# Kernel optimization log

Hardware: AMD Instinct MI355X
Metric: run time of the kernel (lower is better)

The kernel has to match this reference:

```python
import jax, jax.numpy as jnp
import numpy as np

I = 1024
H = 1024
B = 4096
EPS = 1e-5

def layer_norm(x, gamma, beta):
    mu = jnp.mean(x, axis=-1, keepdims=True)
    var = jnp.var(x, axis=-1, keepdims=True)
    return (x - mu) * jax.lax.rsqrt(var + EPS) * gamma + beta

def setup_inputs() -> dict:
    key = jax.random.key(0)
    ks = jax.random.split(key, 5)
    return {
        "input": jax.random.normal(ks[0], (B, I), dtype=jnp.float32),
        "hx": jax.random.normal(ks[1], (B, H), dtype=jnp.float32),
        "cx": jax.random.normal(ks[2], (B, H), dtype=jnp.float32),
        "weight_ih": jax.random.normal(ks[3], (4 * H, I), dtype=jnp.float32),
        "weight_hh": jax.random.normal(ks[4], (4 * H, H), dtype=jnp.float32),
        "gamma_i": jnp.ones((4 * H,), jnp.float32),
        "beta_i": jnp.zeros((4 * H,), jnp.float32),
        "gamma_h": jnp.ones((4 * H,), jnp.float32),
        "beta_h": jnp.zeros((4 * H,), jnp.float32),
        "gamma_c": jnp.ones((H,), jnp.float32),
        "beta_c": jnp.zeros((H,), jnp.float32),
    }

def reference(input, hx, cx, weight_ih, weight_hh,
              gamma_i, beta_i, gamma_h, beta_h, gamma_c, beta_c):
    # igates: [B, 4H]
    igates = layer_norm(jnp.dot(input, weight_ih.T), gamma_i, beta_i)
    hgates = layer_norm(jnp.dot(hx, weight_hh.T), gamma_h, beta_h)
    gates = igates + hgates
    ingate, forgetgate, cellgate, outgate = jnp.split(gates, 4, axis=1)
    ingate = jax.nn.sigmoid(ingate)
    forgetgate = jax.nn.sigmoid(forgetgate)
    cellgate = jnp.tanh(cellgate)
    outgate = jax.nn.sigmoid(outgate)
    cy = layer_norm(forgetgate * cx + ingate * cellgate, gamma_c, beta_c)
    hy = outgate * jnp.tanh(cy)
    return (hy, hy, cy)
```

## Files before the change

kernel.cpp:

```cpp
#include <hip/hip_runtime.h>

#define EPS 1e-5f

typedef unsigned short u16;
typedef __attribute__((ext_vector_type(8))) __bf16 bf16x8;
typedef __attribute__((ext_vector_type(4))) float f32x4;
typedef __attribute__((ext_vector_type(8))) unsigned short ushort8;

__device__ inline float bf2f(u16 h) {
  union { unsigned u; float f; } x; x.u = ((unsigned)h) << 16; return x.f;
}
__device__ inline u16 f2bf(float f) {
  union { float f; unsigned u; } x; x.f = f;
  unsigned r = x.u + 0x7fffu + ((x.u >> 16) & 1u);
  return (u16)(r >> 16);
}
__device__ inline float sigmoidf(float x) { return 1.0f / (1.0f + __expf(-x)); }

__global__ __launch_bounds__(256) void cast4_f32_bf16(
    const float* __restrict__ s0, const float* __restrict__ s1,
    const float* __restrict__ s2, const float* __restrict__ s3,
    u16* __restrict__ d0, u16* __restrict__ d1,
    u16* __restrict__ d2, u16* __restrict__ d3, int n)
{
  const float* s = (blockIdx.y == 0) ? s0 : (blockIdx.y == 1) ? s1 : (blockIdx.y == 2) ? s2 : s3;
  u16*         d = (blockIdx.y == 0) ? d0 : (blockIdx.y == 1) ? d1 : (blockIdx.y == 2) ? d2 : d3;
  int i = (blockIdx.x * 256 + threadIdx.x) * 8;
  if (i >= n) return;
  float4 a = *(const float4*)(s + i);
  float4 b = *(const float4*)(s + i + 4);
  ushort8 o;
  o[0] = f2bf(a.x); o[1] = f2bf(a.y); o[2] = f2bf(a.z); o[3] = f2bf(a.w);
  o[4] = f2bf(b.x); o[5] = f2bf(b.y); o[6] = f2bf(b.z); o[7] = f2bf(b.w);
  *(ushort8*)(d + i) = o;
}

#define MFMA_ __builtin_amdgcn_mfma_f32_16x16x32_bf16

#define STAGE_A(nx, k0) { _Pragma("unroll") for (int i_ = 0; i_ < 4; ++i_) \
  __builtin_amdgcn_global_load_lds( \
      (const __attribute__((address_space(1))) void*)(gA + (size_t)(i_ * 64) * K + (k0)), \
      (__attribute__((address_space(3))) void*)(&sA[nx][(i_ * 512 + (w << 6)) * 8]), 16, 0, 0); }
#define STAGE_B(nx, k0) { _Pragma("unroll") for (int i_ = 0; i_ < 4; ++i_) \
  __builtin_amdgcn_global_load_lds( \
      (const __attribute__((address_space(1))) void*)(gB + (size_t)(i_ * 64) * K + (k0)), \
      (__attribute__((address_space(3))) void*)(&sB[nx][(i_ * 512 + (w << 6)) * 8]), 16, 0, 0); }

#define LDA(mi, sl) (*(const bf16x8*)&sa[(arow + (mi) * 16) * 64 + (sl)])
#define LDB(ni, sl) (*(const bf16x8*)&sb[(brow + (ni) * 16) * 64 + (sl)])

#define MFMA16(m0) \
  __builtin_amdgcn_s_setprio(1); \
  acc[m0 + 0][0] = MFMA_(a0, q0, acc[m0 + 0][0], 0, 0, 0); \
  acc[m0 + 0][1] = MFMA_(a0, q1, acc[m0 + 0][1], 0, 0, 0); \
  acc[m0 + 0][2] = MFMA_(a0, q2, acc[m0 + 0][2], 0, 0, 0); \
  acc[m0 + 0][3] = MFMA_(a0, q3, acc[m0 + 0][3], 0, 0, 0); \
  acc[m0 + 1][0] = MFMA_(a1, q0, acc[m0 + 1][0], 0, 0, 0); \
  acc[m0 + 1][1] = MFMA_(a1, q1, acc[m0 + 1][1], 0, 0, 0); \
  acc[m0 + 1][2] = MFMA_(a1, q2, acc[m0 + 1][2], 0, 0, 0); \
  acc[m0 + 1][3] = MFMA_(a1, q3, acc[m0 + 1][3], 0, 0, 0); \
  acc[m0 + 2][0] = MFMA_(a2, q0, acc[m0 + 2][0], 0, 0, 0); \
  acc[m0 + 2][1] = MFMA_(a2, q1, acc[m0 + 2][1], 0, 0, 0); \
  acc[m0 + 2][2] = MFMA_(a2, q2, acc[m0 + 2][2], 0, 0, 0); \
  acc[m0 + 2][3] = MFMA_(a2, q3, acc[m0 + 2][3], 0, 0, 0); \
  acc[m0 + 3][0] = MFMA_(a3, q0, acc[m0 + 3][0], 0, 0, 0); \
  acc[m0 + 3][1] = MFMA_(a3, q1, acc[m0 + 3][1], 0, 0, 0); \
  acc[m0 + 3][2] = MFMA_(a3, q2, acc[m0 + 3][2], 0, 0, 0); \
  acc[m0 + 3][3] = MFMA_(a3, q3, acc[m0 + 3][3], 0, 0, 0); \
  __builtin_amdgcn_s_setprio(0);

#define PHASE(m0, sl, RB) { \
  bf16x8 a0 = LDA(m0 + 0, sl), a1 = LDA(m0 + 1, sl), a2 = LDA(m0 + 2, sl), a3 = LDA(m0 + 3, sl); \
  if (RB) { q0 = LDB(0, sl); q1 = LDB(1, sl); q2 = LDB(2, sl); q3 = LDB(3, sl); } \
  __builtin_amdgcn_s_barrier(); \
  MFMA16(m0) }

#define PHASE_NOBAR(m0, sl, RB) { \
  bf16x8 a0 = LDA(m0 + 0, sl), a1 = LDA(m0 + 1, sl), a2 = LDA(m0 + 2, sl), a3 = LDA(m0 + 3, sl); \
  if (RB) { q0 = LDB(0, sl); q1 = LDB(1, sl); q2 = LDB(2, sl); q3 = LDB(3, sl); } \
  MFMA16(m0) }

__global__ __launch_bounds__(512, 2) void gemm256_dual(
    const u16* __restrict__ A0, const u16* __restrict__ W0, u16* __restrict__ C0,
    const u16* __restrict__ A1, const u16* __restrict__ W1, u16* __restrict__ C1)
{
  constexpr int K = 1024, N = 4096, NT = 16;

  __shared__ __attribute__((aligned(16))) u16 sA[2][256 * 64];
  __shared__ __attribute__((aligned(16))) u16 sB[2][256 * 64];

  const int b0  = blockIdx.x;
  const int bid = (b0 & 7) * 64 + (b0 >> 3);

  const u16* A  = (bid < 256) ? A0 : A1;
  const u16* Wm = (bid < 256) ? W0 : W1;
  u16*       C  = (bid < 256) ? C0 : C1;
  const int b2 = bid & 255;
  const int bm = (b2 >> 4) << 8;
  const int bn = (b2 & 15) << 8;

  const int tid = threadIdx.x;
  const int l  = tid & 63;
  const int w  = tid >> 6;
  const int wr = w >> 2;
  const int wc = w & 3;

  const int rb   = tid >> 3;
  const int slot = (tid & 7) ^ (rb & 7);
  const u16* gA = A  + (size_t)(bm + rb) * K + slot * 8;
  const u16* gB = Wm + (size_t)(bn + rb) * K + slot * 8;

  const int arow = wr * 128 + (l & 15);
  const int brow = wc * 64 + (l & 15);
  const int sl0 = (((l >> 4) + 0) ^ (l & 7)) * 8;
  const int sl1 = (((l >> 4) + 4) ^ (l & 7)) * 8;

  f32x4 acc[8][4];
#pragma unroll
  for (int i = 0; i < 8; ++i)
#pragma unroll
    for (int j = 0; j < 4; ++j) acc[i][j] = (f32x4){0.f, 0.f, 0.f, 0.f};

  STAGE_A(0, 0)
  STAGE_B(0, 0)

  for (int t = 0; t < NT - 1; ++t) {
    const int cur = t & 1, nxt = cur ^ 1;
    const int kn = (t + 1) << 6;
    const u16* sa = sA[cur];
    const u16* sb = sB[cur];
    bf16x8 q0, q1, q2, q3;

    STAGE_A(nxt, kn)
    asm volatile("s_waitcnt vmcnt(4)" ::: "memory");
    __builtin_amdgcn_s_barrier();
    PHASE_NOBAR(0, sl0, 1)
    __builtin_amdgcn_s_barrier();
    STAGE_B(nxt, kn)
    PHASE(4, sl0, 0)
    __builtin_amdgcn_s_barrier();
    PHASE(0, sl1, 1)
    __builtin_amdgcn_s_barrier();
    PHASE(4, sl1, 0)
  }

  {
    const u16* sa = sA[(NT - 1) & 1];
    const u16* sb = sB[(NT - 1) & 1];
    bf16x8 q0, q1, q2, q3;
    asm volatile("s_waitcnt vmcnt(0)" ::: "memory");
    __builtin_amdgcn_s_barrier();
    PHASE_NOBAR(0, sl0, 1)
    __builtin_amdgcn_s_barrier();
    PHASE(4, sl0, 0)
    __builtin_amdgcn_s_barrier();
    PHASE(0, sl1, 1)
    __builtin_amdgcn_s_barrier();
    PHASE(4, sl1, 0)
  }

  const int ccol = bn + wc * 64 + (l & 15);
  const int crow = bm + wr * 128 + (l >> 4) * 4;
#pragma unroll
  for (int mi = 0; mi < 8; ++mi) {
#pragma unroll
    for (int ni = 0; ni < 4; ++ni) {
      int col = ccol + ni * 16;
#pragma unroll
      for (int r = 0; r < 4; ++r) {
        int row = crow + mi * 16 + r;
        C[(size_t)row * N + col] = f2bf(acc[mi][ni][r]);
      }
    }
  }
}

__global__ __launch_bounds__(256) void lstm_epilogue(
    const u16* __restrict__ ig, const u16* __restrict__ hg,
    const float* __restrict__ cx,
    const float* __restrict__ gi, const float* __restrict__ bi,
    const float* __restrict__ gh, const float* __restrict__ bh,
    const float* __restrict__ gc, const float* __restrict__ bc,
    float* __restrict__ out)
{
  const int b = blockIdx.x;
  const int t = threadIdx.x;
  const u16* igr = ig + (size_t)b * 4096;
  const u16* hgr = hg + (size_t)b * 4096;

  __shared__ float redbuf[16];

  float iv[16], hv[16];
  float s_i = 0.f, q_i = 0.f, s_h = 0.f, q_h = 0.f;
#pragma unroll
  for (int i = 0; i < 16; ++i) {
    float a = bf2f(igr[t + 256 * i]);
    float c = bf2f(hgr[t + 256 * i]);
    iv[i] = a; hv[i] = c;
    s_i += a; q_i += a * a; s_h += c; q_h += c * c;
  }
#pragma unroll
  for (int off = 32; off > 0; off >>= 1) {
    s_i += __shfl_xor(s_i, off);
    q_i += __shfl_xor(q_i, off);
    s_h += __shfl_xor(s_h, off);
    q_h += __shfl_xor(q_h, off);
  }
  {
    int wv = t >> 6;
    if ((t & 63) == 0) {
      redbuf[wv] = s_i; redbuf[wv + 4] = q_i;
      redbuf[wv + 8] = s_h; redbuf[wv + 12] = q_h;
    }
    __syncthreads();
    s_i = redbuf[0] + redbuf[1] + redbuf[2] + redbuf[3];
    q_i = redbuf[4] + redbuf[5] + redbuf[6] + redbuf[7];
    s_h = redbuf[8] + redbuf[9] + redbuf[10] + redbuf[11];
    q_h = redbuf[12] + redbuf[13] + redbuf[14] + redbuf[15];
    __syncthreads();
  }
  const float inv4096 = 1.0f / 4096.0f;
  float mu_i = s_i * inv4096;
  float rs_i = rsqrtf(q_i * inv4096 - mu_i * mu_i + EPS);
  float mu_h = s_h * inv4096;
  float rs_h = rsqrtf(q_h * inv4096 - mu_h * mu_h + EPS);

  float c_pre[4], og[4];
  float s_c = 0.f, q_c = 0.f;
#pragma unroll
  for (int i = 0; i < 4; ++i) {
    int h = t + 256 * i;
    float g_in = ((iv[i]      - mu_i) * rs_i * gi[h]        + bi[h]) +
                 ((hv[i]      - mu_h) * rs_h * gh[h]        + bh[h]);
    float g_fg = ((iv[i + 4]  - mu_i) * rs_i * gi[h + 1024] + bi[h + 1024]) +
                 ((hv[i + 4]  - mu_h) * rs_h * gh[h + 1024] + bh[h + 1024]);
    float g_cl = ((iv[i + 8]  - mu_i) * rs_i * gi[h + 2048] + bi[h + 2048]) +
                 ((hv[i + 8]  - mu_h) * rs_h * gh[h + 2048] + bh[h + 2048]);
    float g_og = ((iv[i + 12] - mu_i) * rs_i * gi[h + 3072] + bi[h + 3072]) +
                 ((hv[i + 12] - mu_h) * rs_h * gh[h + 3072] + bh[h + 3072]);
    float in_s = sigmoidf(g_in);
    float fg_s = sigmoidf(g_fg);
    float cl_t = tanhf(g_cl);
    og[i] = sigmoidf(g_og);
    c_pre[i] = fg_s * cx[(size_t)b * 1024 + h] + in_s * cl_t;
    s_c += c_pre[i]; q_c += c_pre[i] * c_pre[i];
  }
#pragma unroll
  for (int off = 32; off > 0; off >>= 1) {
    s_c += __shfl_xor(s_c, off);
    q_c += __shfl_xor(q_c, off);
  }
  {
    int wv = t >> 6;
    if ((t & 63) == 0) { redbuf[wv] = s_c; redbuf[wv + 4] = q_c; }
    __syncthreads();
    s_c = redbuf[0] + redbuf[1] + redbuf[2] + redbuf[3];
    q_c = redbuf[4] + redbuf[5] + redbuf[6] + redbuf[7];
  }
  const float inv1024 = 1.0f / 1024.0f;
  float mu_c = s_c * inv1024;
  float rs_c = rsqrtf(q_c * inv1024 - mu_c * mu_c + EPS);

  const size_t BH = (size_t)4096 * 1024;
#pragma unroll
  for (int i = 0; i < 4; ++i) {
    int h = t + 256 * i;
    float cy = (c_pre[i] - mu_c) * rs_c * gc[h] + bc[h];
    float hy = og[i] * tanhf(cy);
    size_t o = (size_t)b * 1024 + h;
    out[o] = hy;
    out[BH + o] = hy;
    out[2 * BH + o] = cy;
  }
}

extern "C" void kernel_launch(void* const* d_in, const int* in_sizes, int n_in,
                              void* d_out, int out_size, void* d_ws, size_t ws_size,
                              hipStream_t stream) {
  const float* input = (const float*)d_in[0];
  const float* hx    = (const float*)d_in[1];
  const float* cx    = (const float*)d_in[2];
  const float* wih   = (const float*)d_in[3];
  const float* whh   = (const float*)d_in[4];
  const float* gi    = (const float*)d_in[5];
  const float* bi    = (const float*)d_in[6];
  const float* gh    = (const float*)d_in[7];
  const float* bh    = (const float*)d_in[8];
  const float* gc    = (const float*)d_in[9];
  const float* bc    = (const float*)d_in[10];
  float* out = (float*)d_out;

  char* wsp = (char*)d_ws;
  u16* a_bf  = (u16*)(wsp);
  u16* h_bf  = (u16*)(wsp + ((size_t)8  << 20));
  u16* wi_bf = (u16*)(wsp + ((size_t)16 << 20));
  u16* wh_bf = (u16*)(wsp + ((size_t)24 << 20));
  u16* ig_bf = (u16*)(wsp + ((size_t)32 << 20));
  u16* hg_bf = (u16*)(wsp + ((size_t)64 << 20));

  const int nper = 4096 * 1024;
  dim3 cgrid(nper / 8 / 256, 4);
  cast4_f32_bf16<<<cgrid, 256, 0, stream>>>(input, hx, wih, whh,
                                            a_bf, h_bf, wi_bf, wh_bf, nper);

  gemm256_dual<<<512, 512, 0, stream>>>(a_bf, wi_bf, ig_bf,
                                        h_bf, wh_bf, hg_bf);

  lstm_epilogue<<<4096, 256, 0, stream>>>(ig_bf, hg_bf, cx,
                                          gi, bi, gh, bh, gc, bc, out);
}
```

Before: 125.2 us.

## Halve GEMM K-tile to 32 and restructure staging/compute phases for higher occupancy

The K tile of the dual bf16 GEMM shrinks from 64 to 32, which halves LDS usage per block and doubles the iteration count. Staging of A and B is merged into one macro with a new XOR swizzle for the 32-wide rows. Each iteration now issues its MFMAs in two halves with a single barrier instead of four barrier-separated phases. The launch bound is raised to 4 blocks per CU to get more occupancy and latency hiding, at the cost of register pressure and more loop overhead per FLOP.

```diff
diff --git a/kernel.cpp b/kernel.cpp
--- a/kernel.cpp
+++ b/kernel.cpp
@@ -37,19 +37,20 @@
 
 #define MFMA_ __builtin_amdgcn_mfma_f32_16x16x32_bf16
 
-#define STAGE_A(nx, k0) { _Pragma("unroll") for (int i_ = 0; i_ < 4; ++i_) \
-  __builtin_amdgcn_global_load_lds( \
-      (const __attribute__((address_space(1))) void*)(gA + (size_t)(i_ * 64) * K + (k0)), \
-      (__attribute__((address_space(3))) void*)(&sA[nx][(i_ * 512 + (w << 6)) * 8]), 16, 0, 0); }
-#define STAGE_B(nx, k0) { _Pragma("unroll") for (int i_ = 0; i_ < 4; ++i_) \
-  __builtin_amdgcn_global_load_lds( \
-      (const __attribute__((address_space(1))) void*)(gB + (size_t)(i_ * 64) * K + (k0)), \
-      (__attribute__((address_space(3))) void*)(&sB[nx][(i_ * 512 + (w << 6)) * 8]), 16, 0, 0); }
-
-#define LDA(mi, sl) (*(const bf16x8*)&sa[(arow + (mi) * 16) * 64 + (sl)])
-#define LDB(ni, sl) (*(const bf16x8*)&sb[(brow + (ni) * 16) * 64 + (sl)])
-
-#define MFMA16(m0) \
+#define STAGE(nx, kt) { \
+  _Pragma("unroll") for (int i_ = 0; i_ < 2; ++i_) \
+    __builtin_amdgcn_global_load_lds( \
+        (const __attribute__((address_space(1))) void*)(gA + (size_t)(i_ * 128) * K + (kt)), \
+        (__attribute__((address_space(3))) void*)(&sA[nx][(i_ * 512 + tid) * 8]), 16, 0, 0); \
+  _Pragma("unroll") for (int i_ = 0; i_ < 2; ++i_) \
+    __builtin_amdgcn_global_load_lds( \
+        (const __attribute__((address_space(1))) void*)(gB + (size_t)(i_ * 128) * K + (kt)), \
+        (__attribute__((address_space(3))) void*)(&sB[nx][(i_ * 512 + tid) * 8]), 16, 0, 0); }
+
+#define LDA(mi) (*(const bf16x8*)&sa[(arow + (mi) * 16) * 32 + slr])
+#define LDB(ni) (*(const bf16x8*)&sb[(brow + (ni) * 16) * 32 + slr])
+
+#define MFMA16(m0, a0, a1, a2, a3) \
   __builtin_amdgcn_s_setprio(1); \
   acc[m0 + 0][0] = MFMA_(a0, q0, acc[m0 + 0][0], 0, 0, 0); \
   acc[m0 + 0][1] = MFMA_(a0, q1, acc[m0 + 0][1], 0, 0, 0); \
@@ -69,25 +70,22 @@
   acc[m0 + 3][3] = MFMA_(a3, q3, acc[m0 + 3][3], 0, 0, 0); \
   __builtin_amdgcn_s_setprio(0);
 
-#define PHASE(m0, sl, RB) { \
-  bf16x8 a0 = LDA(m0 + 0, sl), a1 = LDA(m0 + 1, sl), a2 = LDA(m0 + 2, sl), a3 = LDA(m0 + 3, sl); \
-  if (RB) { q0 = LDB(0, sl); q1 = LDB(1, sl); q2 = LDB(2, sl); q3 = LDB(3, sl); } \
+#define TILE_COMPUTE(sa, sb) { \
+  bf16x8 a0 = LDA(0), a1 = LDA(1), a2 = LDA(2), a3 = LDA(3); \
+  q0 = LDB(0); q1 = LDB(1); q2 = LDB(2); q3 = LDB(3); \
+  MFMA16(0, a0, a1, a2, a3) \
+  bf16x8 a4 = LDA(4), a5 = LDA(5), a6 = LDA(6), a7 = LDA(7); \
   __builtin_amdgcn_s_barrier(); \
-  MFMA16(m0) }
-
-#define PHASE_NOBAR(m0, sl, RB) { \
-  bf16x8 a0 = LDA(m0 + 0, sl), a1 = LDA(m0 + 1, sl), a2 = LDA(m0 + 2, sl), a3 = LDA(m0 + 3, sl); \
-  if (RB) { q0 = LDB(0, sl); q1 = LDB(1, sl); q2 = LDB(2, sl); q3 = LDB(3, sl); } \
-  MFMA16(m0) }
-
-__global__ __launch_bounds__(512, 2) void gemm256_dual(
+  MFMA16(4, a4, a5, a6, a7) }
+
+__global__ __launch_bounds__(512, 4) void gemm256_dual(
     const u16* __restrict__ A0, const u16* __restrict__ W0, u16* __restrict__ C0,
     const u16* __restrict__ A1, const u16* __restrict__ W1, u16* __restrict__ C1)
 {
-  constexpr int K = 1024, N = 4096, NT = 16;
-
-  __shared__ __attribute__((aligned(16))) u16 sA[2][256 * 64];
-  __shared__ __attribute__((aligned(16))) u16 sB[2][256 * 64];
+  constexpr int K = 1024, N = 4096, NT = 32;
+
+  __shared__ __attribute__((aligned(16))) u16 sA[2][256 * 32];
+  __shared__ __attribute__((aligned(16))) u16 sB[2][256 * 32];
 
   const int b0  = blockIdx.x;
   const int bid = (b0 & 7) * 64 + (b0 >> 3);
@@ -105,15 +103,15 @@
   const int wr = w >> 2;
   const int wc = w & 3;
 
-  const int rb   = tid >> 3;
-  const int slot = (tid & 7) ^ (rb & 7);
-  const u16* gA = A  + (size_t)(bm + rb) * K + slot * 8;
-  const u16* gB = Wm + (size_t)(bn + rb) * K + slot * 8;
+  const int r0  = tid >> 2;
+  const int ssw = ((tid >> 2) & 3) ^ ((tid >> 4) & 3);
+  const int soff = ((tid & 3) ^ ssw) * 8;
+  const u16* gA = A  + (size_t)(bm + r0) * K + soff;
+  const u16* gB = Wm + (size_t)(bn + r0) * K + soff;
 
   const int arow = wr * 128 + (l & 15);
   const int brow = wc * 64 + (l & 15);
-  const int sl0 = (((l >> 4) + 0) ^ (l & 7)) * 8;
-  const int sl1 = (((l >> 4) + 4) ^ (l & 7)) * 8;
+  const int slr = (((l >> 4) ^ (l & 3) ^ ((l >> 2) & 3))) * 8;
 
   f32x4 acc[8][4];
 #pragma unroll
@@ -121,27 +119,18 @@
 #pragma unroll
     for (int j = 0; j < 4; ++j) acc[i][j] = (f32x4){0.f, 0.f, 0.f, 0.f};
 
-  STAGE_A(0, 0)
-  STAGE_B(0, 0)
+  STAGE(0, 0)
 
   for (int t = 0; t < NT - 1; ++t) {
     const int cur = t & 1, nxt = cur ^ 1;
-    const int kn = (t + 1) << 6;
     const u16* sa = sA[cur];
     const u16* sb = sB[cur];
     bf16x8 q0, q1, q2, q3;
 
-    STAGE_A(nxt, kn)
+    STAGE(nxt, (t + 1) * 32)
     asm volatile("s_waitcnt vmcnt(4)" ::: "memory");
     __builtin_amdgcn_s_barrier();
-    PHASE_NOBAR(0, sl0, 1)
-    __builtin_amdgcn_s_barrier();
-    STAGE_B(nxt, kn)
-    PHASE(4, sl0, 0)
-    __builtin_amdgcn_s_barrier();
-    PHASE(0, sl1, 1)
-    __builtin_amdgcn_s_barrier();
-    PHASE(4, sl1, 0)
+    TILE_COMPUTE(sa, sb)
   }
 
   {
@@ -150,13 +139,7 @@
     bf16x8 q0, q1, q2, q3;
     asm volatile("s_waitcnt vmcnt(0)" ::: "memory");
     __builtin_amdgcn_s_barrier();
-    PHASE_NOBAR(0, sl0, 1)
-    __builtin_amdgcn_s_barrier();
-    PHASE(4, sl0, 0)
-    __builtin_amdgcn_s_barrier();
-    PHASE(0, sl1, 1)
-    __builtin_amdgcn_s_barrier();
-    PHASE(4, sl1, 0)
+    TILE_COMPUTE(sa, sb)
   }
 
   const int ccol = bn + wc * 64 + (l & 15);
```

New measurement: 476.2 us. +280.5%, slower.
